# Optimization experiments

Measured on AMD Instinct MI355X. Metric: run time of the kernel, lower is better.

Reference implementation:

```python
import jax, jax.numpy as jnp
import numpy as np

D_MODEL = 1024
N_HEADS = 16
D_HEAD = 64
LAMBDA_INIT = 0.8  # paper: 0.8 - 0.6*exp(-0.3*(layer-1)); layer=1 -> 0.8


def setup_inputs() -> dict:
    key = jax.random.key(0)
    ks = jax.random.split(key, 6)
    B, S = 2, 2048
    std = 0.02
    x = jax.random.normal(ks[0], (B, S, D_MODEL), dtype=jnp.float32)
    Wq = jax.random.normal(ks[1], (D_MODEL, 2 * N_HEADS * D_HEAD), dtype=jnp.float32) * std
    Wk = jax.random.normal(ks[2], (D_MODEL, 2 * N_HEADS * D_HEAD), dtype=jnp.float32) * std
    Wv = jax.random.normal(ks[3], (D_MODEL, 2 * N_HEADS * D_HEAD), dtype=jnp.float32) * std
    Wo = jax.random.normal(ks[4], (N_HEADS * D_HEAD, D_MODEL), dtype=jnp.float32) * std
    # lambda params initialized to zeros per source (lambda_q1 = zeros(d_head))
    lq1 = jnp.zeros((D_HEAD,), dtype=jnp.float32)
    lk1 = jnp.zeros((D_HEAD,), dtype=jnp.float32)
    lq2 = jnp.zeros((D_HEAD,), dtype=jnp.float32)
    lk2 = jnp.zeros((D_HEAD,), dtype=jnp.float32)
    return {"x": x, "Wq": Wq, "Wk": Wk, "Wv": Wv, "Wo": Wo,
            "lq1": lq1, "lk1": lk1, "lq2": lq2, "lk2": lk2}


def reference(x, Wq, Wk, Wv, Wo, lq1, lk1, lq2, lk2):
    B, S, D = x.shape
    h, dh = N_HEADS, D_HEAD
    # project and split into the two attention-map groups: [B, S, 2, h, dh]
    q = (x @ Wq).reshape(B, S, 2, h, dh)
    k = (x @ Wk).reshape(B, S, 2, h, dh)
    v = (x @ Wv).reshape(B, S, 2, h, dh)
    q1, q2 = q[:, :, 0], q[:, :, 1]  # [B, S, h, dh]
    k1, k2 = k[:, :, 0], k[:, :, 1]
    v1, v2 = v[:, :, 0], v[:, :, 1]

    scale = 1.0 / jnp.sqrt(jnp.asarray(dh, dtype=x.dtype))
    lam = jnp.exp(jnp.dot(lq1, lk1)) - jnp.exp(jnp.dot(lq2, lk2)) + LAMBDA_INIT

    causal = jnp.tril(jnp.ones((S, S), dtype=bool))  # [S, S]
    neg_inf = jnp.asarray(-1e30, dtype=x.dtype)

    s1 = jnp.einsum('bshd,bthd->bhst', q1, k1) * scale
    s2 = jnp.einsum('bshd,bthd->bhst', q2, k2) * scale
    s1 = jnp.where(causal, s1, neg_inf)
    s2 = jnp.where(causal, s2, neg_inf)
    a1 = jax.nn.softmax(s1, axis=-1)
    a2 = jax.nn.softmax(s2, axis=-1)

    # differential attention output per head: A1 @ V1 - lambda * (A2 @ V2)
    o = jnp.einsum('bhst,bthd->bshd', a1, v1) - lam * jnp.einsum('bhst,bthd->bshd', a2, v2)
    o = o.reshape(B, S, h * dh) * (1.0 - LAMBDA_INIT)
    return o @ Wo
```

## Files before the change

kernel.cpp:

```cpp
#include <hip/hip_runtime.h>
#include <hip/hip_bf16.h>

typedef __bf16 bf16_t;
typedef bf16_t bf16x8 __attribute__((ext_vector_type(8)));
typedef float f32x4 __attribute__((ext_vector_type(4)));
typedef float f32x16 __attribute__((ext_vector_type(16)));

static __device__ __forceinline__ f32x4 mfma16(bf16x8 a, bf16x8 b, f32x4 c) {
  return __builtin_amdgcn_mfma_f32_16x16x32_bf16(a, b, c, 0, 0, 0);
}
static __device__ __forceinline__ f32x16 mfma32(bf16x8 a, bf16x8 b, f32x16 c) {
  return __builtin_amdgcn_mfma_f32_32x32x16_bf16(a, b, c, 0, 0, 0);
}

static __device__ __forceinline__ void gload_lds16(const bf16_t* g, bf16_t* l) {
  __builtin_amdgcn_global_load_lds(
      (const __attribute__((address_space(1))) void*)g,
      (__attribute__((address_space(3))) void*)l, 16, 0, 0);
}

static __device__ __forceinline__ unsigned pkbf(float a, float b) {
  union { bf16_t h[2]; unsigned u; } p;
  p.h[0] = (bf16_t)a; p.h[1] = (bf16_t)b;
  return p.u;
}
static __device__ __forceinline__ void pl32swap(unsigned& a, unsigned& b) {
  asm volatile("v_permlane32_swap_b32 %0, %1" : "+v"(a), "+v"(b));
}


__global__ __launch_bounds__(64) void lam_kernel(const float* __restrict__ lq1,
                                                 const float* __restrict__ lk1,
                                                 const float* __restrict__ lq2,
                                                 const float* __restrict__ lk2,
                                                 float* __restrict__ lamp) {
  int l = threadIdx.x;
  float a = lq1[l] * lk1[l];
  float b = lq2[l] * lk2[l];
  #pragma unroll
  for (int msk = 32; msk; msk >>= 1) {
    a += __shfl_xor(a, msk);
    b += __shfl_xor(b, msk);
  }
  if (l == 0) lamp[0] = __expf(a) - __expf(b) + 0.8f;
}

__global__ __launch_bounds__(256) void cvt_x_kernel(const float* __restrict__ x,
                                                    bf16_t* __restrict__ xb) {
  int i = (blockIdx.x * 256 + threadIdx.x) * 4;
  float4 v = *reinterpret_cast<const float4*>(x + i);
  union { bf16_t h[4]; uint2 u; } pk;
  pk.h[0] = (bf16_t)v.x; pk.h[1] = (bf16_t)v.y;
  pk.h[2] = (bf16_t)v.z; pk.h[3] = (bf16_t)v.w;
  *reinterpret_cast<uint2*>(xb + i) = pk.u;
}

__global__ __launch_bounds__(256) void transpose_cvt(const float* __restrict__ W,
                                                     bf16_t* __restrict__ Wt,
                                                     int K, int N) {
  __shared__ float tile[32][33];
  int n0 = blockIdx.x * 32, k0 = blockIdx.y * 32;
  int x = threadIdx.x, y = threadIdx.y;
  #pragma unroll
  for (int i = 0; i < 32; i += 8)
    tile[y + i][x] = W[(size_t)(k0 + y + i) * N + n0 + x];
  __syncthreads();
  #pragma unroll
  for (int i = 0; i < 32; i += 8)
    Wt[(size_t)(n0 + y + i) * K + k0 + x] = (bf16_t)tile[x][y + i];
}


template <typename OutT>
static __device__ __forceinline__ void gemm_bt_body(const bf16_t* __restrict__ A,
                                                    const bf16_t* __restrict__ Bt,
                                                    OutT* __restrict__ C,
                                                    int M, int N, int K,
                                                    bool vtrans) {
  __shared__ bf16_t As[128 * 32];
  __shared__ bf16_t Bs[128 * 32];
  const int tid = threadIdx.x;
  const int w = tid >> 6, lane = tid & 63;
  const int g = lane >> 4, l15 = lane & 15;
  const int wm = w >> 1, wn = w & 1;

  const int nbx = gridDim.x;
  const int idx = blockIdx.y * nbx + blockIdx.x;
  const int qq = (nbx * gridDim.y) >> 3;
  const int sidx = (idx & 7) * qq + (idx >> 3);
  const int rowBase = (sidx / nbx) * 128, colBase = (sidx % nbx) * 128;

  const int c0 = 2 * w, c1 = 2 * w + 1;
  const int srow0 = 16 * c0 + (lane >> 2);
  const int srow1 = 16 * c1 + (lane >> 2);
  const int scol = (lane & 3) * 8;

  f32x4 acc[4][4] = {};

  for (int k0 = 0; k0 < K; k0 += 32) {
    __syncthreads();
    gload_lds16(A + (size_t)(rowBase + srow0) * K + k0 + scol, &As[c0 * 512]);
    gload_lds16(A + (size_t)(rowBase + srow1) * K + k0 + scol, &As[c1 * 512]);
    gload_lds16(Bt + (size_t)(colBase + srow0) * K + k0 + scol, &Bs[c0 * 512]);
    gload_lds16(Bt + (size_t)(colBase + srow1) * K + k0 + scol, &Bs[c1 * 512]);
    __syncthreads();

    bf16x8 bfr[4];
    #pragma unroll
    for (int j = 0; j < 4; ++j)
      bfr[j] = *reinterpret_cast<const bf16x8*>(&Bs[(wn * 64 + j * 16 + l15) * 32 + g * 8]);
    #pragma unroll
    for (int i = 0; i < 4; ++i) {
      bf16x8 afr = *reinterpret_cast<const bf16x8*>(&As[(wm * 64 + i * 16 + l15) * 32 + g * 8]);
      #pragma unroll
      for (int j = 0; j < 4; ++j)
        acc[i][j] = mfma16(afr, bfr[j], acc[i][j]);
    }
  }

  if (vtrans) {
    #pragma unroll
    for (int i = 0; i < 4; ++i) {
      #pragma unroll
      for (int j = 0; j < 4; ++j) {
        int row = rowBase + wm * 64 + i * 16 + 4 * g;
        int col = colBase + wn * 64 + j * 16 + l15;
        int bb = row >> 11, s = row & 2047;
        union { bf16_t h[4]; uint2 u; } pk;
        #pragma unroll
        for (int r = 0; r < 4; ++r) pk.h[r] = (bf16_t)acc[i][j][r];
        *reinterpret_cast<uint2*>(
            (bf16_t*)C + ((size_t)bb * 2048 + col) * 2048 + s) = pk.u;
      }
    }
  } else {
    #pragma unroll
    for (int i = 0; i < 4; ++i) {
      #pragma unroll
      for (int j = 0; j < 4; ++j) {
        int row = rowBase + wm * 64 + i * 16 + 4 * g;
        int col = colBase + wn * 64 + j * 16 + l15;
        #pragma unroll
        for (int r = 0; r < 4; ++r)
          C[(size_t)(row + r) * N + col] = (OutT)acc[i][j][r];
      }
    }
  }
}

__global__ __launch_bounds__(256) void gemm_qkv(const bf16_t* __restrict__ xb,
                                                const bf16_t* __restrict__ Wqt,
                                                const bf16_t* __restrict__ Wkt,
                                                const bf16_t* __restrict__ Wvt,
                                                bf16_t* __restrict__ Q,
                                                bf16_t* __restrict__ K,
                                                bf16_t* __restrict__ Vtg) {
  const bf16_t* Bt = (blockIdx.z == 0) ? Wqt : (blockIdx.z == 1) ? Wkt : Wvt;
  bf16_t* C = (blockIdx.z == 0) ? Q : (blockIdx.z == 1) ? K : Vtg;
  gemm_bt_body<bf16_t>(xb, Bt, C, 4096, 2048, 1024, blockIdx.z == 2);
}

__global__ __launch_bounds__(256) void gemm_out(const bf16_t* __restrict__ Ob,
                                                const bf16_t* __restrict__ Wot,
                                                float* __restrict__ out) {
  gemm_bt_body<float>(Ob, Wot, out, 4096, 1024, 1024, false);
}


__global__ __launch_bounds__(512, 1)
void attn_kernel(const bf16_t* __restrict__ Qg, const bf16_t* __restrict__ Kg,
                 const bf16_t* __restrict__ Vtg, bf16_t* __restrict__ Og,
                 const float* __restrict__ lamp) {
  __shared__ __align__(16) char ldsbuf[65536];
  __shared__ float lsArr[4][2][32];

  const int tid = threadIdx.x;
  const int w = tid >> 6, lane = tid & 63;
  const int l31 = lane & 31, hi = lane >> 5;
  const int sw7 = l31 & 7;
  const int rowg = w & 3, keyh = w >> 2;
  const int bx = blockIdx.x;
  const int p = bx >> 5;
  const int bh = bx & 31;
  const int b = bh >> 4, h = bh & 15;
  const int rowB = b * 2048;
  const float lam = *lamp;
  const float cexp = 0.125f * 1.44269504088896340736f;

  const int lk8 = lane >> 3;
  const int sc8 = (lane & 7) ^ lk8;
  const int lk4 = lane >> 4;
  const int wv = (w - 4) & 3;
  const size_t kOff = (size_t)(rowB + ((w & 1) << 6) + lk8) * 2048 +
                      (w >> 1) * 1024 + h * 64 + sc8 * 8;
  const size_t vOff = ((size_t)b * 2048 + (wv >> 1) * 1024 + h * 64 +
                       ((wv & 1) << 5) + lk4) * 2048;

  auto stage = [&](char* bufb, int j0) {
    if (w < 4) {
      const bf16_t* src = Kg + kOff + (size_t)j0 * 2048;
      char* dst = bufb + w * 8192;
      #pragma unroll
      for (int t = 0; t < 8; ++t)
        gload_lds16(src + (size_t)t * (8 * 2048), (bf16_t*)(dst + t * 1024));
    } else {
      const bf16_t* src = Vtg + vOff + j0;
      char* dst = bufb + 32768 + wv * 8192;
      #pragma unroll
      for (int t = 0; t < 8; ++t) {
        int sc16 = (lane & 15) ^ (((t & 1) << 2) + lk4);
        gload_lds16(src + (size_t)t * (4 * 2048) + sc16 * 8,
                    (bf16_t*)(dst + t * 1024));
      }
    }
  };

  f32x16 o[2][2];
  float ls[2];
  bf16x8 qf[2][4];

  auto finalize = [&](int q0, char* scratch) {
    float* sf = (float*)scratch;
    #pragma unroll
    for (int rd = 0; rd < 4; ++rd) {
      const int comp = rd >> 1, db = rd & 1;
      __syncthreads();
      if (w >= 4) {
        float* bp = sf + (size_t)((w - 4) * 64 + lane) * 17;
        #pragma unroll
        for (int e = 0; e < 16; ++e) bp[e] = o[comp][db][e];
        if (db == 0) bp[16] = ls[comp];
      }
      __syncthreads();
      if (w < 4) {
        const float* bp = sf + (size_t)(w * 64 + lane) * 17;
        #pragma unroll
        for (int e = 0; e < 16; ++e) o[comp][db][e] += bp[e];
        if (db == 0) ls[comp] += bp[16];
      }
    }
    __syncthreads();
    if (w < 4) {
      #pragma unroll
      for (int comp = 0; comp < 2; ++comp) {
        float tot = ls[comp] + __shfl_xor(ls[comp], 32);
        lsArr[w][comp][l31] = 1.f / tot;
      }
    }
    __syncthreads();
    if (w < 4) {
      #pragma unroll
      for (int e = 0; e < 16; ++e) {
        int ql = (e & 3) + 8 * (e >> 2) + 4 * hi;
        float i1 = lsArr[w][0][ql];
        float i2 = lsArr[w][1][ql] * lam;
        int row = rowB + q0 + w * 32 + ql;
        size_t rb = (size_t)row * 1024 + h * 64 + l31;
        Og[rb]      = (bf16_t)((o[0][0][e] * i1 - o[1][0][e] * i2) * 0.2f);
        Og[rb + 32] = (bf16_t)((o[0][1][e] * i1 - o[1][1][e] * i2) * 0.2f);
      }
    }
  };

  #pragma unroll 1
  for (int i = 0; i <= 16; ++i) {
    const int q0 = (i > p ? 15 - p : p) << 7;
    const int j0 = (i > p ? i - p - 1 : i) << 7;

    __syncthreads();
    stage(ldsbuf, j0);

    if (i == 0 || i == p + 1) {
      #pragma unroll
      for (int comp = 0; comp < 2; ++comp)
        #pragma unroll
        for (int s = 0; s < 4; ++s)
          qf[comp][s] = *reinterpret_cast<const bf16x8*>(
              Qg + (size_t)(rowB + q0 + rowg * 32 + l31) * 2048 + comp * 1024 +
              h * 64 + s * 16 + hi * 8);
      #pragma unroll
      for (int comp = 0; comp < 2; ++comp) {
        o[comp][0] = (f32x16)0.f;
        o[comp][1] = (f32x16)0.f;
        ls[comp] = 0.f;
      }
    }

    __syncthreads();

    const char* bufb = (const char*)ldsbuf;
    const int qg = q0 + rowg * 32 + l31;
    const bool active = (j0 + keyh * 64) <= (q0 + rowg * 32 + 31);
    if (active) {
      const bool maskt = (j0 + keyh * 64 + 63) > (q0 + rowg * 32);
      #pragma unroll
      for (int comp = 0; comp < 2; ++comp) {
        const char* Kb = bufb + comp * 16384 + keyh * 64 * 128;
        const char* Vb = bufb + 32768 + comp * 16384;
        #pragma unroll
        for (int kb = 0; kb < 2; ++kb) {
          f32x16 sA = {};
          #pragma unroll
          for (int s = 0; s < 4; ++s) {
            int xo = ((2 * s + hi) ^ sw7) << 4;
            bf16x8 kf = *reinterpret_cast<const bf16x8*>(
                Kb + (kb * 32 + l31) * 128 + xo);
            sA = mfma32(kf, qf[comp][s], sA);
          }
          float pv[16];
          #pragma unroll
          for (int e = 0; e < 16; ++e) {
            float v = __builtin_exp2f(sA[e] * cexp);
            if (maskt) {
              int krow = (e & 3) + 8 * (e >> 2) + 4 * hi;
              if (j0 + keyh * 64 + kb * 32 + krow > qg) v = 0.f;
            }
            pv[e] = v;
            ls[comp] += v;
          }
          bf16x8 pa[2];
          #pragma unroll
          for (int sp = 0; sp < 2; ++sp) {
            unsigned u0 = pkbf(pv[8 * sp + 0], pv[8 * sp + 1]);
            unsigned u1 = pkbf(pv[8 * sp + 2], pv[8 * sp + 3]);
            unsigned v0 = pkbf(pv[8 * sp + 4], pv[8 * sp + 5]);
            unsigned v1 = pkbf(pv[8 * sp + 6], pv[8 * sp + 7]);
            pl32swap(u0, v0);
            pl32swap(u1, v1);
            union { uint4 u; bf16x8 f; } cvt;
            cvt.u = make_uint4(u0, u1, v0, v1);
            pa[sp] = cvt.f;
          }
          #pragma unroll
          for (int sp = 0; sp < 2; ++sp) {
            int s = kb * 2 + sp;
            int sl = ((keyh * 8) | ((2 * s + hi) ^ sw7)) << 4;
            bf16x8 vf0 = *reinterpret_cast<const bf16x8*>(Vb + l31 * 256 + sl);
            bf16x8 vf1 = *reinterpret_cast<const bf16x8*>(Vb + (32 + l31) * 256 + sl);
            o[comp][0] = mfma32(pa[sp], vf0, o[comp][0]);
            o[comp][1] = mfma32(pa[sp], vf1, o[comp][1]);
          }
        }
      }
    }

    if (i == p || i == 16) finalize(q0, ldsbuf);
  }
}


extern "C" void kernel_launch(void* const* d_in, const int* in_sizes, int n_in,
                              void* d_out, int out_size, void* d_ws, size_t ws_size,
                              hipStream_t stream) {
  const float* x   = (const float*)d_in[0];
  const float* Wq  = (const float*)d_in[1];
  const float* Wk  = (const float*)d_in[2];
  const float* Wv  = (const float*)d_in[3];
  const float* Wo  = (const float*)d_in[4];
  const float* lq1 = (const float*)d_in[5];
  const float* lk1 = (const float*)d_in[6];
  const float* lq2 = (const float*)d_in[7];
  const float* lk2 = (const float*)d_in[8];
  float* out = (float*)d_out;

  char* ws = (char*)d_ws;
  size_t off = 0;
  auto alloc = [&](size_t bytes) -> char* {
    char* p = ws + off;
    off += (bytes + 255) & ~(size_t)255;
    return p;
  };
  bf16_t* xb  = (bf16_t*)alloc((size_t)4096 * 1024 * 2);
  bf16_t* Wqt = (bf16_t*)alloc((size_t)2048 * 1024 * 2);
  bf16_t* Wkt = (bf16_t*)alloc((size_t)2048 * 1024 * 2);
  bf16_t* Wvt = (bf16_t*)alloc((size_t)2048 * 1024 * 2);
  bf16_t* Wot = (bf16_t*)alloc((size_t)1024 * 1024 * 2);
  bf16_t* Qb  = (bf16_t*)alloc((size_t)4096 * 2048 * 2);
  bf16_t* Kb  = (bf16_t*)alloc((size_t)4096 * 2048 * 2);
  bf16_t* Vtg = (bf16_t*)alloc((size_t)4096 * 2048 * 2);
  bf16_t* Ob  = (bf16_t*)alloc((size_t)4096 * 1024 * 2);
  float*  lamp = (float*)alloc(256);

  lam_kernel<<<1, 64, 0, stream>>>(lq1, lk1, lq2, lk2, lamp);
  cvt_x_kernel<<<4096, 256, 0, stream>>>(x, xb);
  transpose_cvt<<<dim3(64, 32), dim3(32, 8), 0, stream>>>(Wq, Wqt, 1024, 2048);
  transpose_cvt<<<dim3(64, 32), dim3(32, 8), 0, stream>>>(Wk, Wkt, 1024, 2048);
  transpose_cvt<<<dim3(64, 32), dim3(32, 8), 0, stream>>>(Wv, Wvt, 1024, 2048);
  transpose_cvt<<<dim3(32, 32), dim3(32, 8), 0, stream>>>(Wo, Wot, 1024, 1024);
  gemm_qkv<<<dim3(16, 32, 3), 256, 0, stream>>>(xb, Wqt, Wkt, Wvt, Qb, Kb, Vtg);
  attn_kernel<<<256, 512, 0, stream>>>(Qb, Kb, Vtg, Ob, lamp);
  gemm_out<<<dim3(8, 32), 256, 0, stream>>>(Ob, Wot, out);
}
```

Baseline: 199.3 us.

## Split attention blocks across components and row halves, combine outputs separately

```diff
diff --git a/kernel.cpp b/kernel.cpp
--- a/kernel.cpp
+++ b/kernel.cpp
@@ -70,6 +70,21 @@
     Wt[(size_t)(n0 + y + i) * K + k0 + x] = (bf16_t)tile[x][y + i];
 }
 
+__global__ __launch_bounds__(256) void combine_kernel(const bf16_t* __restrict__ Ob1,
+                                                      const bf16_t* __restrict__ Ob2,
+                                                      bf16_t* __restrict__ Ob,
+                                                      const float* __restrict__ lamp) {
+  int i = (blockIdx.x * 256 + threadIdx.x) * 8;
+  const float lam = lamp[0];
+  bf16x8 a = *reinterpret_cast<const bf16x8*>(Ob1 + i);
+  bf16x8 c = *reinterpret_cast<const bf16x8*>(Ob2 + i);
+  bf16x8 r;
+  #pragma unroll
+  for (int j = 0; j < 8; ++j)
+    r[j] = (bf16_t)(0.2f * ((float)a[j] - lam * (float)c[j]));
+  *reinterpret_cast<bf16x8*>(Ob + i) = r;
+}
+
 
 template <typename OutT>
 static __device__ __forceinline__ void gemm_bt_body(const bf16_t* __restrict__ A,
@@ -167,37 +182,39 @@
 }
 
 
-__global__ __launch_bounds__(512, 1)
+__global__ __launch_bounds__(256, 1)
 void attn_kernel(const bf16_t* __restrict__ Qg, const bf16_t* __restrict__ Kg,
-                 const bf16_t* __restrict__ Vtg, bf16_t* __restrict__ Og,
-                 const float* __restrict__ lamp) {
-  __shared__ __align__(16) char ldsbuf[65536];
-  __shared__ float lsArr[4][2][32];
+                 const bf16_t* __restrict__ Vtg, bf16_t* __restrict__ Ob1,
+                 bf16_t* __restrict__ Ob2) {
+  __shared__ __align__(16) char ldsbuf[32768];
+  __shared__ float lsArr[2][32];
 
   const int tid = threadIdx.x;
   const int w = tid >> 6, lane = tid & 63;
   const int l31 = lane & 31, hi = lane >> 5;
   const int sw7 = l31 & 7;
-  const int rowg = w & 3, keyh = w >> 2;
+  const int rowg = w & 1, keyh = w >> 1;
   const int bx = blockIdx.x;
-  const int p = bx >> 5;
-  const int bh = bx & 31;
+  const int comp = bx & 1;
+  const int rhalf = (bx >> 1) & 1;
+  const int bh = (bx >> 2) & 31;
+  const int p = bx >> 7;
   const int b = bh >> 4, h = bh & 15;
   const int rowB = b * 2048;
-  const float lam = *lamp;
   const float cexp = 0.125f * 1.44269504088896340736f;
+  bf16_t* __restrict__ Obc = comp ? Ob2 : Ob1;
 
   const int lk8 = lane >> 3;
   const int sc8 = (lane & 7) ^ lk8;
   const int lk4 = lane >> 4;
-  const int wv = (w - 4) & 3;
+  const int wv = (w - 2) & 1;
   const size_t kOff = (size_t)(rowB + ((w & 1) << 6) + lk8) * 2048 +
-                      (w >> 1) * 1024 + h * 64 + sc8 * 8;
-  const size_t vOff = ((size_t)b * 2048 + (wv >> 1) * 1024 + h * 64 +
-                       ((wv & 1) << 5) + lk4) * 2048;
+                      comp * 1024 + h * 64 + sc8 * 8;
+  const size_t vOff = ((size_t)b * 2048 + comp * 1024 + h * 64 +
+                       (wv << 5) + lk4) * 2048;
 
   auto stage = [&](char* bufb, int j0) {
-    if (w < 4) {
+    if (w < 2) {
       const bf16_t* src = Kg + kOff + (size_t)j0 * 2048;
       char* dst = bufb + w * 8192;
       #pragma unroll
@@ -205,7 +222,7 @@
         gload_lds16(src + (size_t)t * (8 * 2048), (bf16_t*)(dst + t * 1024));
     } else {
       const bf16_t* src = Vtg + vOff + j0;
-      char* dst = bufb + 32768 + wv * 8192;
+      char* dst = bufb + 16384 + wv * 8192;
       #pragma unroll
       for (int t = 0; t < 8; ++t) {
         int sc16 = (lane & 15) ^ (((t & 1) << 2) + lk4);
@@ -215,49 +232,44 @@
     }
   };
 
-  f32x16 o[2][2];
-  float ls[2];
-  bf16x8 qf[2][4];
+  f32x16 o[2];
+  float ls;
+  bf16x8 qf[4];
 
   auto finalize = [&](int q0, char* scratch) {
     float* sf = (float*)scratch;
     #pragma unroll
-    for (int rd = 0; rd < 4; ++rd) {
-      const int comp = rd >> 1, db = rd & 1;
+    for (int db = 0; db < 2; ++db) {
       __syncthreads();
-      if (w >= 4) {
-        float* bp = sf + (size_t)((w - 4) * 64 + lane) * 17;
-        #pragma unroll
-        for (int e = 0; e < 16; ++e) bp[e] = o[comp][db][e];
-        if (db == 0) bp[16] = ls[comp];
+      if (w >= 2) {
+        float* bp = sf + (size_t)((w - 2) * 64 + lane) * 17;
+        #pragma unroll
+        for (int e = 0; e < 16; ++e) bp[e] = o[db][e];
+        if (db == 0) bp[16] = ls;
       }
       __syncthreads();
-      if (w < 4) {
+      if (w < 2) {
         const float* bp = sf + (size_t)(w * 64 + lane) * 17;
         #pragma unroll
-        for (int e = 0; e < 16; ++e) o[comp][db][e] += bp[e];
-        if (db == 0) ls[comp] += bp[16];
-      }
-    }
-    __syncthreads();
-    if (w < 4) {
-      #pragma unroll
-      for (int comp = 0; comp < 2; ++comp) {
-        float tot = ls[comp] + __shfl_xor(ls[comp], 32);
-        lsArr[w][comp][l31] = 1.f / tot;
-      }
-    }
-    __syncthreads();
-    if (w < 4) {
+        for (int e = 0; e < 16; ++e) o[db][e] += bp[e];
+        if (db == 0) ls += bp[16];
+      }
+    }
+    __syncthreads();
+    if (w < 2) {
+      float tot = ls + __shfl_xor(ls, 32);
+      lsArr[w][l31] = 1.f / tot;
+    }
+    __syncthreads();
+    if (w < 2) {
       #pragma unroll
       for (int e = 0; e < 16; ++e) {
         int ql = (e & 3) + 8 * (e >> 2) + 4 * hi;
-        float i1 = lsArr[w][0][ql];
-        float i2 = lsArr[w][1][ql] * lam;
-        int row = rowB + q0 + w * 32 + ql;
+        float inv = lsArr[w][ql];
+        int row = rowB + q0 + rhalf * 64 + w * 32 + ql;
         size_t rb = (size_t)row * 1024 + h * 64 + l31;
-        Og[rb]      = (bf16_t)((o[0][0][e] * i1 - o[1][0][e] * i2) * 0.2f);
-        Og[rb + 32] = (bf16_t)((o[0][1][e] * i1 - o[1][1][e] * i2) * 0.2f);
+        Obc[rb]      = (bf16_t)(o[0][e] * inv);
+        Obc[rb + 32] = (bf16_t)(o[1][e] * inv);
       }
     }
   };
@@ -272,74 +284,67 @@
 
     if (i == 0 || i == p + 1) {
       #pragma unroll
-      for (int comp = 0; comp < 2; ++comp)
-        #pragma unroll
-        for (int s = 0; s < 4; ++s)
-          qf[comp][s] = *reinterpret_cast<const bf16x8*>(
-              Qg + (size_t)(rowB + q0 + rowg * 32 + l31) * 2048 + comp * 1024 +
-              h * 64 + s * 16 + hi * 8);
-      #pragma unroll
-      for (int comp = 0; comp < 2; ++comp) {
-        o[comp][0] = (f32x16)0.f;
-        o[comp][1] = (f32x16)0.f;
-        ls[comp] = 0.f;
-      }
+      for (int s = 0; s < 4; ++s)
+        qf[s] = *reinterpret_cast<const bf16x8*>(
+            Qg + (size_t)(rowB + q0 + rhalf * 64 + rowg * 32 + l31) * 2048 +
+            comp * 1024 + h * 64 + s * 16 + hi * 8);
+      o[0] = (f32x16)0.f;
+      o[1] = (f32x16)0.f;
+      ls = 0.f;
     }
 
     __syncthreads();
 
     const char* bufb = (const char*)ldsbuf;
-    const int qg = q0 + rowg * 32 + l31;
-    const bool active = (j0 + keyh * 64) <= (q0 + rowg * 32 + 31);
+    const int rowbase = q0 + rhalf * 64 + rowg * 32;
+    const int qg = rowbase + l31;
+    const bool active = (j0 + keyh * 64) <= (rowbase + 31);
     if (active) {
-      const bool maskt = (j0 + keyh * 64 + 63) > (q0 + rowg * 32);
-      #pragma unroll
-      for (int comp = 0; comp < 2; ++comp) {
-        const char* Kb = bufb + comp * 16384 + keyh * 64 * 128;
-        const char* Vb = bufb + 32768 + comp * 16384;
-        #pragma unroll
-        for (int kb = 0; kb < 2; ++kb) {
-          f32x16 sA = {};
-          #pragma unroll
-          for (int s = 0; s < 4; ++s) {
-            int xo = ((2 * s + hi) ^ sw7) << 4;
-            bf16x8 kf = *reinterpret_cast<const bf16x8*>(
-                Kb + (kb * 32 + l31) * 128 + xo);
-            sA = mfma32(kf, qf[comp][s], sA);
+      const bool maskt = (j0 + keyh * 64 + 63) > rowbase;
+      const char* Kb = bufb + keyh * 8192;
+      const char* Vb = bufb + 16384;
+      #pragma unroll
+      for (int kb = 0; kb < 2; ++kb) {
+        f32x16 sA = {};
+        #pragma unroll
+        for (int s = 0; s < 4; ++s) {
+          int xo = ((2 * s + hi) ^ sw7) << 4;
+          bf16x8 kf = *reinterpret_cast<const bf16x8*>(
+              Kb + (kb * 32 + l31) * 128 + xo);
+          sA = mfma32(kf, qf[s], sA);
+        }
+        float pv[16];
+        #pragma unroll
+        for (int e = 0; e < 16; ++e) {
+          float v = __builtin_exp2f(sA[e] * cexp);
+          if (maskt) {
+            int krow = (e & 3) + 8 * (e >> 2) + 4 * hi;
+            if (j0 + keyh * 64 + kb * 32 + krow > qg) v = 0.f;
           }
-          float pv[16];
-          #pragma unroll
-          for (int e = 0; e < 16; ++e) {
-            float v = __builtin_exp2f(sA[e] * cexp);
-            if (maskt) {
-              int krow = (e & 3) + 8 * (e >> 2) + 4 * hi;
-              if (j0 + keyh * 64 + kb * 32 + krow > qg) v = 0.f;
-            }
-            pv[e] = v;
-            ls[comp] += v;
-          }
-          bf16x8 pa[2];
-          #pragma unroll
-          for (int sp = 0; sp < 2; ++sp) {
-            unsigned u0 = pkbf(pv[8 * sp + 0], pv[8 * sp + 1]);
-            unsigned u1 = pkbf(pv[8 * sp + 2], pv[8 * sp + 3]);
-            unsigned v0 = pkbf(pv[8 * sp + 4], pv[8 * sp + 5]);
-            unsigned v1 = pkbf(pv[8 * sp + 6], pv[8 * sp + 7]);
-            pl32swap(u0, v0);
-            pl32swap(u1, v1);
-            union { uint4 u; bf16x8 f; } cvt;
-            cvt.u = make_uint4(u0, u1, v0, v1);
-            pa[sp] = cvt.f;
-          }
-          #pragma unroll
-          for (int sp = 0; sp < 2; ++sp) {
-            int s = kb * 2 + sp;
-            int sl = ((keyh * 8) | ((2 * s + hi) ^ sw7)) << 4;
-            bf16x8 vf0 = *reinterpret_cast<const bf16x8*>(Vb + l31 * 256 + sl);
-            bf16x8 vf1 = *reinterpret_cast<const bf16x8*>(Vb + (32 + l31) * 256 + sl);
-            o[comp][0] = mfma32(pa[sp], vf0, o[comp][0]);
-            o[comp][1] = mfma32(pa[sp], vf1, o[comp][1]);
-          }
+          pv[e] = v;
+          ls += v;
+        }
+        bf16x8 pa[2];
+        #pragma unroll
+        for (int sp = 0; sp < 2; ++sp) {
+          unsigned u0 = pkbf(pv[8 * sp + 0], pv[8 * sp + 1]);
+          unsigned u1 = pkbf(pv[8 * sp + 2], pv[8 * sp + 3]);
+          unsigned v0 = pkbf(pv[8 * sp + 4], pv[8 * sp + 5]);
+          unsigned v1 = pkbf(pv[8 * sp + 6], pv[8 * sp + 7]);
+          pl32swap(u0, v0);
+          pl32swap(u1, v1);
+          union { uint4 u; bf16x8 f; } cvt;
+          cvt.u = make_uint4(u0, u1, v0, v1);
+          pa[sp] = cvt.f;
+        }
+        #pragma unroll
+        for (int sp = 0; sp < 2; ++sp) {
+          int s = kb * 2 + sp;
+          int sl = ((keyh * 8) | ((2 * s + hi) ^ sw7)) << 4;
+          bf16x8 vf0 = *reinterpret_cast<const bf16x8*>(Vb + l31 * 256 + sl);
+          bf16x8 vf1 = *reinterpret_cast<const bf16x8*>(Vb + (32 + l31) * 256 + sl);
+          o[0] = mfma32(pa[sp], vf0, o[0]);
+          o[1] = mfma32(pa[sp], vf1, o[1]);
         }
       }
     }
@@ -381,6 +386,9 @@
   bf16_t* Ob  = (bf16_t*)alloc((size_t)4096 * 1024 * 2);
   float*  lamp = (float*)alloc(256);
 
+  bf16_t* Ob1 = xb;
+  bf16_t* Ob2 = Wqt;
+
   lam_kernel<<<1, 64, 0, stream>>>(lq1, lk1, lq2, lk2, lamp);
   cvt_x_kernel<<<4096, 256, 0, stream>>>(x, xb);
   transpose_cvt<<<dim3(64, 32), dim3(32, 8), 0, stream>>>(Wq, Wqt, 1024, 2048);
@@ -388,6 +396,7 @@
   transpose_cvt<<<dim3(64, 32), dim3(32, 8), 0, stream>>>(Wv, Wvt, 1024, 2048);
   transpose_cvt<<<dim3(32, 32), dim3(32, 8), 0, stream>>>(Wo, Wot, 1024, 1024);
   gemm_qkv<<<dim3(16, 32, 3), 256, 0, stream>>>(xb, Wqt, Wkt, Wvt, Qb, Kb, Vtg);
-  attn_kernel<<<256, 512, 0, stream>>>(Qb, Kb, Vtg, Ob, lamp);
+  attn_kernel<<<1024, 256, 0, stream>>>(Qb, Kb, Vtg, Ob1, Ob2);
+  combine_kernel<<<2048, 256, 0, stream>>>(Ob1, Ob2, Ob, lamp);
   gemm_out<<<dim3(8, 32), 256, 0, stream>>>(Ob, Wot, out);
 }
```

New measurement: 216.9 us. 1.09x slower.
